# Kernel optimization log

Hardware: AMD Instinct MI355X
Metric: run time of the kernel (lower is better)

Reference implementation:

```python
import jax, jax.numpy as jnp
import numpy as np

LLR_CLIP = 20.0   # allowed_llr_range(abs=20)
QMAX = 7.5        # decoder_qms_qbit = 5 -> round(x*2)/2, clip +/-7.5


def _quantize_ste(x):
    # straight-through quantizer: forward = quantized, grad flows through clipped x
    q = jnp.clip(jnp.round(x * 2.0) / 2.0, -QMAX, QMAX)
    xc = jnp.clip(x, -QMAX, QMAX)
    return xc + jax.lax.stop_gradient(q - xc)


def _decode(xa, cn_weights, vn_idx, cn_idx, shifts, M):
    # xa: (B, Z, N) channel LLRs; messages live on lifted edges (B, Z, E)
    B, Z, N = xa.shape
    E = vn_idx.shape[0]
    iters = cn_weights.shape[0]

    zidx = jnp.arange(Z)
    lift = (zidx[:, None] + shifts[None, :]) % Z    # VN-domain -> CN-domain cyclic shift per edge
    unlift = (zidx[:, None] - shifts[None, :]) % Z  # inverse shift
    lift_b = jnp.broadcast_to(lift[None], (B, Z, E))
    unlift_b = jnp.broadcast_to(unlift[None], (B, Z, E))

    V = jax.nn.one_hot(vn_idx, N, dtype=xa.dtype)   # (E, N) edge->VN incidence (= W_output / W_skipconn2even)
    eids = jnp.arange(E)
    llr_e = xa[:, :, vn_idx]                        # per-edge channel LLR (B, Z, E)

    c2v = jnp.zeros((B, Z, E), xa.dtype)
    for it in range(iters):
        # --- VN update (odd layer): extrinsic sum + channel LLR, clipped ---
        tot = jnp.einsum('bze,en->bzn', c2v, V)                 # per-VN sum of incoming c2v
        v2c = jnp.clip(llr_e + tot[:, :, vn_idx] - c2v, -LLR_CLIP, LLR_CLIP)

        # --- lift to CN domain (Lift_Matrix1) ---
        m = jnp.take_along_axis(v2c, lift_b, axis=1)            # (B, Z, E)
        mt = m.transpose(2, 0, 1).reshape(E, B * Z)             # edges leading for segment ops

        # --- CN update (even layer): extrinsic min-sum via two-min trick ---
        a = jnp.abs(mt)
        neg = (mt < 0).astype(jnp.int32)
        min1 = jax.ops.segment_min(a, cn_idx, num_segments=M)               # (M, B*Z)
        ismin = a == min1[cn_idx]
        first = jax.ops.segment_min(jnp.where(ismin, eids[:, None], E),
                                    cn_idx, num_segments=M)                 # tie-break by edge id
        isfirst = eids[:, None] == first[cn_idx]
        min2 = jax.ops.segment_min(jnp.where(isfirst, jnp.inf, a),
                                   cn_idx, num_segments=M)
        ext_min = jnp.where(isfirst, min2[cn_idx], min1[cn_idx])
        negtot = jax.ops.segment_sum(neg, cn_idx, num_segments=M)
        sgn = (1 - 2 * ((negtot[cn_idx] - neg) % 2)).astype(mt.dtype)       # extrinsic sign product

        msg = _quantize_ste(cn_weights[it] * sgn * ext_min)     # per-iteration scalar CN weight + QMS quantize

        # --- unlift back to VN domain (Lift_Matrix2) ---
        mc = msg.reshape(E, B, Z).transpose(1, 2, 0)
        c2v = jnp.take_along_axis(mc, unlift_b, axis=1)

    # marginal output LLRs (W_output): channel + all incoming c2v, shape (B, N*Z)
    out = xa + jnp.einsum('bze,en->bzn', c2v, V)
    return out.transpose(0, 2, 1).reshape(B, N * Z)


def setup_inputs() -> dict:
    key = jax.random.key(0)
    B, Z, N, M, dc = 32, 384, 68, 46, 7
    E = M * dc  # 322
    k1, k2, k3 = jax.random.split(key, 3)
    xa = jax.random.normal(k1, (B, Z, N), dtype=jnp.float32) * 4.0
    cn_weights = jnp.ones((8,), jnp.float32)
    cn_idx = jnp.repeat(jnp.arange(M), dc)                      # regular CN degree 7
    vn_idx = jax.random.randint(k2, (E,), 0, N)
    shifts = jax.random.randint(k3, (E,), 0, Z)
    return {"xa": xa, "cn_weights": cn_weights, "vn_idx": vn_idx,
            "cn_idx": cn_idx, "shifts": shifts, "M": M}


def reference(xa, cn_weights, vn_idx, cn_idx, shifts, M):
    return _decode(xa, cn_weights, vn_idx, cn_idx, shifts, M)
```

## Files before the change

### kernel.cpp

```cpp
#include <hip/hip_runtime.h>

#define B_   32
#define Z_   384
#define N_   68
#define M_   46
#define DC_  7
#define E_   (M_ * DC_)
#define ZN   (Z_ * N_)
#define ZM   (Z_ * M_)
#define MSB  (DC_ * ZM)

#define XAT_OFF   0
#define LT_OFF    (B_ * ZN)
#define MSG_OFF   (2 * B_ * ZN)
#define MSG_INTS  ((B_ * MSB + 3) / 4)
#define EVS_OFF   (MSG_OFF + MSG_INTS)
#define OFFS_OFF  (EVS_OFF + E_)
#define LST_OFF   (OFFS_OFF + N_ + 1)
#define WS_INTS   (LST_OFF + E_)


__global__ __launch_bounds__(384)
void k_pre_tables(const float* __restrict__ xa,
                  const int* __restrict__ vn_idx, const int* __restrict__ shifts,
                  int* __restrict__ ws, float* __restrict__ xat_dst)
{
    const int tid = threadIdx.x;
    if (blockIdx.x == B_ * 6) {
        __shared__ int vnl[E_];
        __shared__ int shl[E_];
        __shared__ int offs[N_ + 1];
        if (tid < E_) { vnl[tid] = vn_idx[tid]; shl[tid] = shifts[tid]; }
        __syncthreads();
        if (tid < N_) {
            int c = 0;
            for (int e = 0; e < E_; ++e) c += (vnl[e] == tid);
            offs[tid + 1] = c;
        }
        if (tid == 0) offs[0] = 0;
        __syncthreads();
        if (tid == 0) { for (int n = 0; n < N_; ++n) offs[n + 1] += offs[n]; }
        __syncthreads();
        if (tid < E_) {
            ws[EVS_OFF + tid] = (vnl[tid] * Z_ << 9) | shl[tid];
        }
        if (tid < N_ + 1) ws[OFFS_OFF + tid] = offs[tid];
        if (tid < N_) {
            int p = offs[tid];
            for (int e = 0; e < E_; ++e) {
                if (vnl[e] == tid) {
                    int m = e / DC_, j = e - m * DC_;
                    ws[LST_OFF + p++] = ((j * ZM + m * Z_) << 9) | shl[e];
                }
            }
        }
        return;
    }
    __shared__ float tile[N_ * 65];
    const int x = blockIdx.x & 7;
    const int k = blockIdx.x >> 3;
    const int b = x + 8 * (k & 3);
    const int t = k >> 2;
    const int z0 = t * 64;
    const float* src = xa + (size_t)b * ZN + (size_t)z0 * N_;
    for (int i = tid; i < 64 * N_; i += 384) {
        int r = i / N_, n = i - r * N_;
        tile[n * 65 + r] = src[i];
    }
    __syncthreads();
    float* dst = xat_dst + (size_t)b * ZN + z0;
    for (int i = tid; i < 64 * N_; i += 384) {
        int n = i >> 6, zl = i & 63;
        dst[n * Z_ + zl] = tile[n * 65 + zl];
    }
}

__global__ __launch_bounds__(384)
void k_passB(const float* __restrict__ cw, const int* __restrict__ ws_tbl,
             signed char* __restrict__ msg, const float* __restrict__ src_g,
             int it, int use_init)
{
    __shared__ int cevs[DC_];
    const int x = blockIdx.x & 7;
    const int k = blockIdx.x >> 3;
    const int b = x + 8 * (k & 3);
    const int m = k >> 2;
    const int z = threadIdx.x;
    if (z < DC_) cevs[z] = ws_tbl[EVS_OFF + m * DC_ + z];
    __syncthreads();

    const float* src = src_g + (size_t)b * ZN;
    signed char* mp = msg + (size_t)b * MSB + m * Z_ + z;
    const float w = cw[it];

    float m1 = 1e30f, m2 = 1e30f;
    int f = 0, negb = 0;
    #pragma unroll
    for (int j = 0; j < DC_; ++j) {
        int rec = cevs[j];
        int s = rec & 511;
        int zr = z + s; if (zr >= Z_) zr -= Z_;
        int c2 = use_init ? 0 : (int)mp[j * ZM];
        float v = src[(rec >> 9) + zr] - 0.5f * (float)c2;
        v = fminf(fmaxf(v, -20.0f), 20.0f);
        negb |= (v < 0.0f) << j;
        float a = fabsf(v);
        if (a < m1) { m2 = m1; m1 = a; f = j; }
        else if (a < m2) { m2 = a; }
    }
    float r1 = fminf(fmaxf(rintf(w * m1 * 2.0f), -15.0f), 15.0f);
    float r2 = fminf(fmaxf(rintf(w * m2 * 2.0f), -15.0f), 15.0f);
    const int q1 = (int)r1, q2 = (int)r2;
    const int par = __popc(negb);
    #pragma unroll
    for (int j = 0; j < DC_; ++j) {
        int q  = (j == f) ? q2 : q1;
        int sj = (par - ((negb >> j) & 1)) & 1;
        mp[j * ZM] = (signed char)(sj ? -q : q);
    }
}

__global__ __launch_bounds__(384)
void k_passA(const float* __restrict__ xat, const int* __restrict__ ws_tbl,
             const signed char* __restrict__ msg, float* __restrict__ dst)
{
    __shared__ int vlist[16];
    __shared__ int s_cnt;
    const int x = blockIdx.x & 7;
    const int k = blockIdx.x >> 3;
    const int b = x + 8 * (k & 3);
    const int n = k >> 2;
    const int tid = threadIdx.x;
    const int o = ws_tbl[OFFS_OFF + n];
    const int e = ws_tbl[OFFS_OFF + n + 1];
    if (tid == 0) s_cnt = e - o;
    if (tid < e - o && tid < 16) vlist[tid] = ws_tbl[LST_OFF + o + tid];
    __syncthreads();

    const int z = tid;
    const signed char* mb = msg + (size_t)b * MSB;
    const int cnt = s_cnt;
    int t2 = 0;
    for (int q = 0; q < cnt; ++q) {
        int rec = (q < 16) ? vlist[q] : ws_tbl[LST_OFF + o + q];
        int s = rec & 511;
        int zs = z - s; if (zs < 0) zs += Z_;
        t2 += (int)mb[(rec >> 9) + zs];
    }
    dst[(size_t)b * ZN + n * Z_ + z] =
        xat[(size_t)b * ZN + n * Z_ + z] + 0.5f * (float)t2;
}

#define INIT_STATE ((16u << 10) | (16u << 15))
__device__ __forceinline__ int decode2(unsigned st, int j) {
    int neg   = (st >> j) & 1;
    int q1    = (int)((st >> 10) & 31) - 16;
    int q2    = (int)((st >> 15) & 31) - 16;
    int first = (int)((st >> 7) & 7);
    int q     = (j == first) ? q2 : q1;
    int par   = (__popc(st & 127u) - neg) & 1;
    return par ? -q : q;
}

__global__ __launch_bounds__(1024)
void ldpc_decode_kernel(const float* __restrict__ xa,
                        const float* __restrict__ cw,
                        const int*   __restrict__ vn_idx,
                        const int*   __restrict__ shifts,
                        float* out, int iters)
{
    __shared__ short tot[ZN];
    __shared__ int   evs[E_];
    __shared__ int   offs[N_ + 1];
    __shared__ int   lists[E_];
    __shared__ float wlds[8];

    const int tid = threadIdx.x;
    const int b   = blockIdx.x;
    const float* xab = xa + (size_t)b * ZN;
    float* outb = out + (size_t)b * ZN;
    int* stateg = (int*)outb;

    if (tid < E_) evs[tid] = vn_idx[tid] | (shifts[tid] << 7);
    if (tid < iters && tid < 8) wlds[tid] = cw[tid];
    __syncthreads();
    if (tid < N_) {
        int c = 0;
        for (int e = 0; e < E_; ++e) c += ((evs[e] & 127) == tid);
        offs[tid + 1] = c;
    }
    if (tid == 0) offs[0] = 0;
    __syncthreads();
    if (tid == 0) { for (int n = 0; n < N_; ++n) offs[n + 1] += offs[n]; }
    __syncthreads();
    if (tid < N_) {
        int p = offs[tid];
        for (int e = 0; e < E_; ++e) {
            int rec = evs[e];
            if ((rec & 127) == tid) {
                int s = rec >> 7;
                lists[p++] = s | ((e / DC_) << 9) | ((e % DC_) << 15);
            }
        }
    }
    __syncthreads();

    for (int i = tid; i < ZM; i += 1024) stateg[i] = (int)INIT_STATE;
    __syncthreads();

    for (int it = 0; it < iters; ++it) {
        for (int i = tid; i < ZN; i += 1024) {
            int z = i / N_, n = i - z * N_, t2 = 0;
            int kend = offs[n + 1];
            for (int k = offs[n]; k < kend; ++k) {
                int rec = lists[k];
                int s = rec & 511, m = (rec >> 9) & 63, j = rec >> 15;
                int zs = z - s; if (zs < 0) zs += Z_;
                t2 += decode2((unsigned)stateg[zs * M_ + m], j);
            }
            tot[i] = (short)t2;
        }
        __syncthreads();
        const float w = wlds[it];
        for (int i = tid; i < ZM; i += 1024) {
            int z = i / M_, m = i - z * M_;
            unsigned st = (unsigned)stateg[i];
            float m1 = 1e30f, m2 = 1e30f;
            int f = 0, negb = 0;
            #pragma unroll
            for (int j = 0; j < DC_; ++j) {
                int rec = evs[m * DC_ + j];
                int vn = rec & 127, s = rec >> 7;
                int zr = z + s; if (zr >= Z_) zr -= Z_;
                int c2 = decode2(st, j);
                int idx = zr * N_ + vn;
                float v = (xab[idx] + 0.5f * (float)tot[idx]) - 0.5f * (float)c2;
                v = fminf(fmaxf(v, -20.0f), 20.0f);
                negb |= (v < 0.0f) << j;
                float a = fabsf(v);
                if (a < m1) { m2 = m1; m1 = a; f = j; }
                else if (a < m2) { m2 = a; }
            }
            float r1 = fminf(fmaxf(rintf(w * m1 * 2.0f), -15.0f), 15.0f);
            float r2 = fminf(fmaxf(rintf(w * m2 * 2.0f), -15.0f), 15.0f);
            stateg[i] = (int)(unsigned)(negb | (f << 7) | (((int)r1 + 16) << 10) | (((int)r2 + 16) << 15));
        }
        __syncthreads();
    }

    for (int i = tid; i < ZN; i += 1024) {
        int z = i / N_, n = i - z * N_, t2 = 0;
        int kend = offs[n + 1];
        for (int k = offs[n]; k < kend; ++k) {
            int rec = lists[k];
            int s = rec & 511, m = (rec >> 9) & 63, j = rec >> 15;
            int zs = z - s; if (zs < 0) zs += Z_;
            t2 += decode2((unsigned)stateg[zs * M_ + m], j);
        }
        tot[i] = (short)t2;
    }
    __syncthreads();
    for (int i = tid; i < ZN; i += 1024) {
        int n = i / Z_, z = i - n * Z_;
        outb[i] = xab[z * N_ + n] + 0.5f * (float)tot[z * N_ + n];
    }
}

extern "C" void kernel_launch(void* const* d_in, const int* in_sizes, int n_in,
                              void* d_out, int out_size, void* d_ws, size_t ws_size,
                              hipStream_t stream) {
    const float* xa = (const float*)d_in[0];
    const float* cw = (const float*)d_in[1];
    const int* vn   = (const int*)d_in[2];
    const int* sh   = (const int*)d_in[4];
    int iters = in_sizes[1];
    float* outp = (float*)d_out;

    if (ws_size >= (size_t)WS_INTS * sizeof(int)) {
        int*         ws  = (int*)d_ws;
        float*       xat = (float*)d_ws + XAT_OFF;
        float*       lt  = (float*)d_ws + LT_OFF;
        signed char* msg = (signed char*)(ws + MSG_OFF);

        if (iters == 0) {
            hipLaunchKernelGGL(k_pre_tables, dim3(B_ * 6 + 1), dim3(384), 0, stream,
                               xa, vn, sh, ws, outp);
            return;
        }
        hipLaunchKernelGGL(k_pre_tables, dim3(B_ * 6 + 1), dim3(384), 0, stream,
                           xa, vn, sh, ws, xat);
        hipLaunchKernelGGL(k_passB, dim3(B_ * M_), dim3(384), 0, stream,
                           cw, ws, msg, xat, 0, 1);
        for (int it = 1; it < iters; ++it) {
            hipLaunchKernelGGL(k_passA, dim3(B_ * N_), dim3(384), 0, stream,
                               xat, ws, msg, lt);
            hipLaunchKernelGGL(k_passB, dim3(B_ * M_), dim3(384), 0, stream,
                               cw, ws, msg, lt, it, 0);
        }
        hipLaunchKernelGGL(k_passA, dim3(B_ * N_), dim3(384), 0, stream,
                           xat, ws, msg, outp);
    } else {
        hipLaunchKernelGGL(ldpc_decode_kernel, dim3(B_), dim3(1024), 0, stream,
                           xa, cw, vn, sh, outp, iters);
    }
}
```

Before: 201.5 us.

## Fuse all decoder passes into one persistent per-batch kernel

Replaces the sequence of table/transposition, CN-pass and VN-pass launches with a single kernel that runs one 1024-thread block per batch and loops over iterations with block barriers. Tables are rebuilt in shared memory by each block instead of in a separate launch. This removes many kernel launches and inter-kernel gaps, but it shrinks the grid to 32 blocks, leaving most compute units idle for the gather-heavy passes.

```diff
diff --git a/kernel.cpp b/kernel.cpp
--- a/kernel.cpp
+++ b/kernel.cpp
@@ -14,141 +14,123 @@
 #define LT_OFF    (B_ * ZN)
 #define MSG_OFF   (2 * B_ * ZN)
 #define MSG_INTS  ((B_ * MSB + 3) / 4)
-#define EVS_OFF   (MSG_OFF + MSG_INTS)
-#define OFFS_OFF  (EVS_OFF + E_)
-#define LST_OFF   (OFFS_OFF + N_ + 1)
-#define WS_INTS   (LST_OFF + E_)
-
-
-__global__ __launch_bounds__(384)
-void k_pre_tables(const float* __restrict__ xa,
-                  const int* __restrict__ vn_idx, const int* __restrict__ shifts,
-                  int* __restrict__ ws, float* __restrict__ xat_dst)
+#define WS_INTS   (MSG_OFF + MSG_INTS)
+
+
+__global__ __launch_bounds__(1024)
+void k_all(const float* __restrict__ xa, const float* __restrict__ cw,
+           const int* __restrict__ vn_idx, const int* __restrict__ shifts,
+           float* __restrict__ xat_g, float* __restrict__ lt_g,
+           signed char* __restrict__ msg_g, float* __restrict__ out, int iters)
 {
+    __shared__ int   evs[E_];
+    __shared__ int   lists[E_];
+    __shared__ int   offs[N_ + 1];
+    __shared__ float wlds[8];
+    __shared__ float tile[N_ * 65];
+
     const int tid = threadIdx.x;
-    if (blockIdx.x == B_ * 6) {
-        __shared__ int vnl[E_];
-        __shared__ int shl[E_];
-        __shared__ int offs[N_ + 1];
-        if (tid < E_) { vnl[tid] = vn_idx[tid]; shl[tid] = shifts[tid]; }
-        __syncthreads();
-        if (tid < N_) {
-            int c = 0;
-            for (int e = 0; e < E_; ++e) c += (vnl[e] == tid);
-            offs[tid + 1] = c;
-        }
-        if (tid == 0) offs[0] = 0;
-        __syncthreads();
-        if (tid == 0) { for (int n = 0; n < N_; ++n) offs[n + 1] += offs[n]; }
-        __syncthreads();
-        if (tid < E_) {
-            ws[EVS_OFF + tid] = (vnl[tid] * Z_ << 9) | shl[tid];
-        }
-        if (tid < N_ + 1) ws[OFFS_OFF + tid] = offs[tid];
-        if (tid < N_) {
-            int p = offs[tid];
-            for (int e = 0; e < E_; ++e) {
-                if (vnl[e] == tid) {
-                    int m = e / DC_, j = e - m * DC_;
-                    ws[LST_OFF + p++] = ((j * ZM + m * Z_) << 9) | shl[e];
-                }
-            }
-        }
-        return;
-    }
-    __shared__ float tile[N_ * 65];
-    const int x = blockIdx.x & 7;
-    const int k = blockIdx.x >> 3;
-    const int b = x + 8 * (k & 3);
-    const int t = k >> 2;
-    const int z0 = t * 64;
-    const float* src = xa + (size_t)b * ZN + (size_t)z0 * N_;
-    for (int i = tid; i < 64 * N_; i += 384) {
-        int r = i / N_, n = i - r * N_;
-        tile[n * 65 + r] = src[i];
-    }
-    __syncthreads();
-    float* dst = xat_dst + (size_t)b * ZN + z0;
-    for (int i = tid; i < 64 * N_; i += 384) {
-        int n = i >> 6, zl = i & 63;
-        dst[n * Z_ + zl] = tile[n * 65 + zl];
-    }
-}
-
-__global__ __launch_bounds__(384)
-void k_passB(const float* __restrict__ cw, const int* __restrict__ ws_tbl,
-             signed char* __restrict__ msg, const float* __restrict__ src_g,
-             int it, int use_init)
-{
-    __shared__ int cevs[DC_];
-    const int x = blockIdx.x & 7;
-    const int k = blockIdx.x >> 3;
-    const int b = x + 8 * (k & 3);
-    const int m = k >> 2;
-    const int z = threadIdx.x;
-    if (z < DC_) cevs[z] = ws_tbl[EVS_OFF + m * DC_ + z];
-    __syncthreads();
-
-    const float* src = src_g + (size_t)b * ZN;
-    signed char* mp = msg + (size_t)b * MSB + m * Z_ + z;
-    const float w = cw[it];
-
-    float m1 = 1e30f, m2 = 1e30f;
-    int f = 0, negb = 0;
-    #pragma unroll
-    for (int j = 0; j < DC_; ++j) {
-        int rec = cevs[j];
-        int s = rec & 511;
-        int zr = z + s; if (zr >= Z_) zr -= Z_;
-        int c2 = use_init ? 0 : (int)mp[j * ZM];
-        float v = src[(rec >> 9) + zr] - 0.5f * (float)c2;
-        v = fminf(fmaxf(v, -20.0f), 20.0f);
-        negb |= (v < 0.0f) << j;
-        float a = fabsf(v);
-        if (a < m1) { m2 = m1; m1 = a; f = j; }
-        else if (a < m2) { m2 = a; }
-    }
-    float r1 = fminf(fmaxf(rintf(w * m1 * 2.0f), -15.0f), 15.0f);
-    float r2 = fminf(fmaxf(rintf(w * m2 * 2.0f), -15.0f), 15.0f);
-    const int q1 = (int)r1, q2 = (int)r2;
-    const int par = __popc(negb);
-    #pragma unroll
-    for (int j = 0; j < DC_; ++j) {
-        int q  = (j == f) ? q2 : q1;
-        int sj = (par - ((negb >> j) & 1)) & 1;
-        mp[j * ZM] = (signed char)(sj ? -q : q);
-    }
-}
-
-__global__ __launch_bounds__(384)
-void k_passA(const float* __restrict__ xat, const int* __restrict__ ws_tbl,
-             const signed char* __restrict__ msg, float* __restrict__ dst)
-{
-    __shared__ int vlist[16];
-    __shared__ int s_cnt;
-    const int x = blockIdx.x & 7;
-    const int k = blockIdx.x >> 3;
-    const int b = x + 8 * (k & 3);
-    const int n = k >> 2;
-    const int tid = threadIdx.x;
-    const int o = ws_tbl[OFFS_OFF + n];
-    const int e = ws_tbl[OFFS_OFF + n + 1];
-    if (tid == 0) s_cnt = e - o;
-    if (tid < e - o && tid < 16) vlist[tid] = ws_tbl[LST_OFF + o + tid];
-    __syncthreads();
-
-    const int z = tid;
-    const signed char* mb = msg + (size_t)b * MSB;
-    const int cnt = s_cnt;
-    int t2 = 0;
-    for (int q = 0; q < cnt; ++q) {
-        int rec = (q < 16) ? vlist[q] : ws_tbl[LST_OFF + o + q];
-        int s = rec & 511;
-        int zs = z - s; if (zs < 0) zs += Z_;
-        t2 += (int)mb[(rec >> 9) + zs];
-    }
-    dst[(size_t)b * ZN + n * Z_ + z] =
-        xat[(size_t)b * ZN + n * Z_ + z] + 0.5f * (float)t2;
+    const int b   = blockIdx.x;
+
+    int* vnl = (int*)tile;
+    int* shl = vnl + E_;
+    if (tid < E_) { vnl[tid] = vn_idx[tid]; shl[tid] = shifts[tid]; }
+    if (tid < 8) wlds[tid] = cw[tid];
+    __syncthreads();
+    if (tid < N_) {
+        int c = 0;
+        for (int e = 0; e < E_; ++e) c += (vnl[e] == tid);
+        offs[tid + 1] = c;
+    }
+    if (tid == 0) offs[0] = 0;
+    __syncthreads();
+    if (tid == 0) { for (int n = 0; n < N_; ++n) offs[n + 1] += offs[n]; }
+    __syncthreads();
+    if (tid < E_) evs[tid] = (vnl[tid] * Z_ << 9) | shl[tid];
+    if (tid < N_) {
+        int p = offs[tid];
+        for (int e = 0; e < E_; ++e) {
+            if (vnl[e] == tid) {
+                int m = e / DC_, j = e - m * DC_;
+                lists[p++] = ((j * ZM + m * Z_) << 9) | shl[e];
+            }
+        }
+    }
+    __syncthreads();
+
+    const float* xab = xa + (size_t)b * ZN;
+    float* tdst = ((iters == 0) ? out : xat_g) + (size_t)b * ZN;
+    for (int t = 0; t < 6; ++t) {
+        const int z0 = t * 64;
+        const float* src = xab + (size_t)z0 * N_;
+        for (int i = tid; i < 64 * N_; i += 1024) {
+            int r = i / N_, n = i - r * N_;
+            tile[n * 65 + r] = src[i];
+        }
+        __syncthreads();
+        for (int i = tid; i < 64 * N_; i += 1024) {
+            int n = i >> 6, zl = i & 63;
+            tdst[n * Z_ + z0 + zl] = tile[n * 65 + zl];
+        }
+        __syncthreads();
+    }
+    if (iters == 0) return;
+
+    const float* xb = xat_g + (size_t)b * ZN;
+    float*       lb = lt_g + (size_t)b * ZN;
+    signed char* mb = msg_g + (size_t)b * MSB;
+
+    for (int it = 0; it < iters; ++it) {
+        const float* src = (it == 0) ? xb : lb;
+        const float w = wlds[it];
+        const int use_init = (it == 0);
+        for (int l = tid; l < ZM; l += 1024) {
+            const int m = l / Z_;
+            const int z = l - m * Z_;
+            float m1 = 1e30f, m2 = 1e30f;
+            int f = 0, negb = 0;
+            #pragma unroll
+            for (int j = 0; j < DC_; ++j) {
+                int rec = evs[m * DC_ + j];
+                int s = rec & 511;
+                int zr = z + s; if (zr >= Z_) zr -= Z_;
+                int c2 = use_init ? 0 : (int)mb[j * ZM + l];
+                float v = src[(rec >> 9) + zr] - 0.5f * (float)c2;
+                v = fminf(fmaxf(v, -20.0f), 20.0f);
+                negb |= (v < 0.0f) << j;
+                float a = fabsf(v);
+                if (a < m1) { m2 = m1; m1 = a; f = j; }
+                else if (a < m2) { m2 = a; }
+            }
+            float r1 = fminf(fmaxf(rintf(w * m1 * 2.0f), -15.0f), 15.0f);
+            float r2 = fminf(fmaxf(rintf(w * m2 * 2.0f), -15.0f), 15.0f);
+            const int q1 = (int)r1, q2 = (int)r2;
+            const int par = __popc(negb);
+            #pragma unroll
+            for (int j = 0; j < DC_; ++j) {
+                int q  = (j == f) ? q2 : q1;
+                int sj = (par - ((negb >> j) & 1)) & 1;
+                mb[j * ZM + l] = (signed char)(sj ? -q : q);
+            }
+        }
+        __syncthreads();
+
+        float* dst = (it == iters - 1) ? (out + (size_t)b * ZN) : lb;
+        for (int l = tid; l < ZN; l += 1024) {
+            const int n = l / Z_;
+            const int z = l - n * Z_;
+            const int o = offs[n], e = offs[n + 1];
+            int t2 = 0;
+            for (int k = o; k < e; ++k) {
+                int rec = lists[k];
+                int s = rec & 511;
+                int zs = z - s; if (zs < 0) zs += Z_;
+                t2 += (int)mb[(rec >> 9) + zs];
+            }
+            dst[l] = xb[l] + 0.5f * (float)t2;
+        }
+        __syncthreads();
+    }
 }
 
 #define INIT_STATE ((16u << 10) | (16u << 15))
@@ -282,23 +264,8 @@
         float*       lt  = (float*)d_ws + LT_OFF;
         signed char* msg = (signed char*)(ws + MSG_OFF);
 
-        if (iters == 0) {
-            hipLaunchKernelGGL(k_pre_tables, dim3(B_ * 6 + 1), dim3(384), 0, stream,
-                               xa, vn, sh, ws, outp);
-            return;
-        }
-        hipLaunchKernelGGL(k_pre_tables, dim3(B_ * 6 + 1), dim3(384), 0, stream,
-                           xa, vn, sh, ws, xat);
-        hipLaunchKernelGGL(k_passB, dim3(B_ * M_), dim3(384), 0, stream,
-                           cw, ws, msg, xat, 0, 1);
-        for (int it = 1; it < iters; ++it) {
-            hipLaunchKernelGGL(k_passA, dim3(B_ * N_), dim3(384), 0, stream,
-                               xat, ws, msg, lt);
-            hipLaunchKernelGGL(k_passB, dim3(B_ * M_), dim3(384), 0, stream,
-                               cw, ws, msg, lt, it, 0);
-        }
-        hipLaunchKernelGGL(k_passA, dim3(B_ * N_), dim3(384), 0, stream,
-                           xat, ws, msg, outp);
+        hipLaunchKernelGGL(k_all, dim3(B_), dim3(1024), 0, stream,
+                           xa, cw, vn, sh, xat, lt, msg, outp, iters);
     } else {
         hipLaunchKernelGGL(ldpc_decode_kernel, dim3(B_), dim3(1024), 0, stream,
                            xa, cw, vn, sh, outp, iters);
```

New measurement: 619.2 us. +207.3%, slower.
